# Kernel optimization log

Hardware: AMD Instinct MI355X
Metric: run time of the kernel (lower is better)

The kernel has to match this reference:

```python
import jax, jax.numpy as jnp
import numpy as np
from jax import lax

B, C1, IN_CH, OUT_CH, H1, W1 = 2, 64, 128, 64, 128, 128
BN_EPS = 1e-5


def conv3x3(x, w, b=None):
    # x: (N,C,H,W), w: (O,I,3,3), padding=1, stride=1 (matches nn.Conv2d)
    y = lax.conv_general_dilated(x, w, (1, 1), ((1, 1), (1, 1)),
                                 dimension_numbers=('NCHW', 'OIHW', 'NCHW'))
    return y if b is None else y + b[None, :, None, None]


def bn_relu(x, g, b):
    # training-mode BatchNorm2d (batch statistics over N,H,W) followed by ReLU
    m = x.mean((0, 2, 3), keepdims=True)
    v = x.var((0, 2, 3), keepdims=True)
    return jax.nn.relu((x - m) * lax.rsqrt(v + BN_EPS) * g[None, :, None, None]
                       + b[None, :, None, None])


def deform_offset(x, off_w):
    # ConvOffset2D: learn 2 offsets per pixel per channel, bilinear-gather input.
    Bc, C, H, W = x.shape
    offsets = conv3x3(x, off_w)                      # (B, 2C, H, W)
    off = offsets.reshape(Bc * C, H, W, 2)           # same flat reinterpretation as torch .view
    xf = x.reshape(Bc * C, H, W)
    gy, gx = jnp.meshgrid(jnp.arange(H, dtype=x.dtype),
                          jnp.arange(W, dtype=x.dtype), indexing='ij')
    cy = jnp.clip(off[..., 0] + gy, 0.0, H - 1)      # clamp per-axis like th_batch_map_coordinates
    cx = jnp.clip(off[..., 1] + gx, 0.0, W - 1)
    y0f, x0f = jnp.floor(cy), jnp.floor(cx)
    y0 = y0f.astype(jnp.int32); y1 = jnp.ceil(cy).astype(jnp.int32)
    x0 = x0f.astype(jnp.int32); x1c = jnp.ceil(cx).astype(jnp.int32)
    bidx = jnp.arange(Bc * C)[:, None, None]
    v00 = xf[bidx, y0, x0]; v10 = xf[bidx, y1, x0]
    v01 = xf[bidx, y0, x1c]; v11 = xf[bidx, y1, x1c]
    wy = cy - y0f; wx = cx - x0f
    vt = v00 + (v10 - v00) * wy                      # interp along H
    vb = v01 + (v11 - v01) * wy
    return (vt + (vb - vt) * wx).reshape(Bc, C, H, W)


def setup_inputs() -> dict:
    key = jax.random.key(0)
    ks = jax.random.split(key, 8)
    f = jnp.float32
    x1 = jax.random.normal(ks[0], (B, C1, H1, W1), f)
    x2 = jax.random.normal(ks[1], (B, C1, 2 * H1, 2 * W1), f)
    up_w = jax.random.normal(ks[2], (C1, C1, 2, 2), f) * 0.05   # torch IOHW layout
    up_b = jnp.zeros((C1,), f)
    off_w = jax.random.normal(ks[3], (2 * IN_CH, IN_CH, 3, 3), f) * 0.01  # init_normal_stddev
    c1_w = jax.random.normal(ks[4], (OUT_CH, IN_CH, 3, 3), f) * 0.05
    c1_b = jnp.zeros((OUT_CH,), f)
    g1 = jnp.ones((OUT_CH,), f); b1 = jnp.zeros((OUT_CH,), f)
    c2_w = jax.random.normal(ks[5], (OUT_CH, OUT_CH, 3, 3), f) * 0.05
    c2_b = jnp.zeros((OUT_CH,), f)
    g2 = jnp.ones((OUT_CH,), f); b2 = jnp.zeros((OUT_CH,), f)
    return dict(x1=x1, x2=x2, up_w=up_w, up_b=up_b, off_w=off_w,
                c1_w=c1_w, c1_b=c1_b, g1=g1, b1=b1,
                c2_w=c2_w, c2_b=c2_b, g2=g2, b2=b2)


def reference(x1, x2, up_w, up_b, off_w, c1_w, c1_b, g1, b1, c2_w, c2_b, g2, b2):
    # ConvTranspose2d(k=2, s=2): each input pixel expands to a 2x2 block
    Bx, Ci, H, W = x1.shape
    up = jnp.einsum('bihw,iokl->bohkwl', x1, up_w).reshape(Bx, up_w.shape[1], 2 * H, 2 * W)
    up = up + up_b[None, :, None, None]
    # pad skip connection to match (zero here; kept for faithfulness; torch pads W by diffX, H by diffY)
    dX = up.shape[2] - x2.shape[2]
    dY = up.shape[3] - x2.shape[3]
    x2p = jnp.pad(x2, ((0, 0), (0, 0), (dY // 2, dY // 2), (dX // 2, dX // 2)))
    xcat = jnp.concatenate([x2p, up], axis=1)        # (B, IN_CH, 2H, 2W)
    xd = deform_offset(xcat, off_w)
    h = bn_relu(conv3x3(xd, c1_w, c1_b), g1, b1)
    return bn_relu(conv3x3(h, c2_w, c2_b), g2, b2)
```

## Files before the change

### kernel.cpp

```cpp
#include <hip/hip_runtime.h>
#include <hip/hip_bf16.h>


typedef short short8 __attribute__((ext_vector_type(8)));
typedef short short4v __attribute__((ext_vector_type(4)));
typedef float f32x4 __attribute__((ext_vector_type(4)));

__device__ unsigned char g_ws[201u << 20] __attribute__((aligned(256)));
__device__ float g_st[256];

#define OFF_XCAT 0u
#define OFF_OFF  (36u << 20)
#define OFF_XD   (100u << 20)
#define OFF_C1O  (134u << 20)
#define OFF_H1   (150u << 20)
#define OFF_C2O  (168u << 20)
#define OFF_WO   (184u << 20)
#define OFF_W1   ((184u << 20) + 589824u)
#define OFF_W2   ((184u << 20) + 737280u)
#define OFF_XPU  (185u << 20)

#define XROW 264
#define XRSH (XROW * 128)

__device__ __forceinline__ float b2f(__hip_bfloat16 v) { return __bfloat162float(v); }
__device__ __forceinline__ short f2b(float v) {
  __hip_bfloat16 h = __float2bfloat16(v); short s; __builtin_memcpy(&s, &h, 2); return s;
}
__device__ __forceinline__ float s2f(short s) {
  __hip_bfloat16 h; __builtin_memcpy(&h, &s, 2); return __bfloat162float(h);
}
__device__ __forceinline__ void gload_lds16(const void* g, void* l) {
  __builtin_amdgcn_global_load_lds(
      (const __attribute__((address_space(1))) void*)g,
      (__attribute__((address_space(3))) void*)l, 16, 0, 0);
}

__device__ __forceinline__ void halo_zero(short* base, int C, int cshift, int u) {
  const int cg = u & ((1 << cshift) - 1);
  const int rest = u >> cshift;
  const int p = rest % 2576, b = rest / 2576;
  int row, col;
  if (p < 264) { row = 0; col = p; }
  else if (p < 528) { row = 257; col = p - 264; }
  else { int q = p - 528; row = 1 + (q >> 3); int cs = q & 7; col = cs ? 256 + cs : 0; }
  short8 z = {};
  *(short8*)(base + (((size_t)(b * 258) + row) * XROW + col) * C + cg * 8) = z;
}

__global__ __launch_bounds__(256)
void k_prep(const float* __restrict__ offw, const float* __restrict__ c1w,
            const float* __restrict__ c2w) {
  const int fid = blockIdx.x * 256 + threadIdx.x;
  if (blockIdx.x == 0) g_st[threadIdx.x] = 0.f;
  __hip_bfloat16* Wo = (__hip_bfloat16*)(g_ws + OFF_WO);
  __hip_bfloat16* W1 = (__hip_bfloat16*)(g_ws + OFF_W1);
  __hip_bfloat16* W2 = (__hip_bfloat16*)(g_ws + OFF_W2);
  if (fid < 294912) {
    int ic = fid & 127, rest = fid >> 7, oc = rest & 255, tap = rest >> 8;
    Wo[fid] = __float2bfloat16(offw[(oc * 128 + ic) * 9 + tap]);
  } else if (fid < 368640) {
    int l = fid - 294912;
    int ic = l & 127, rest = l >> 7, oc = rest & 63, tap = rest >> 6;
    W1[l] = __float2bfloat16(c1w[(oc * 128 + ic) * 9 + tap]);
  } else if (fid < 405504) {
    int l = fid - 368640;
    int ic = l & 63, rest = l >> 6, oc = rest & 63, tap = rest >> 6;
    W2[l] = __float2bfloat16(c2w[(oc * 64 + ic) * 9 + tap]);
  } else {
    int u = fid - 405504;
    if (u < 82432) halo_zero((short*)(g_ws + OFF_XCAT), 128, 4, u);
    else if (u < 164864) halo_zero((short*)(g_ws + OFF_XD), 128, 4, u - 82432);
    else halo_zero((short*)(g_ws + OFF_H1), 64, 3, u - 164864);
  }
}

__global__ __launch_bounds__(256)
void k_xpose(const float* __restrict__ x2) {
  __shared__ short T[256][72];
  const int t = threadIdx.x;
  const int h = blockIdx.x & 255, b = blockIdx.x >> 8;
  const float* src = x2 + (size_t)(b * 64) * 65536 + h * 256;
  for (int rep = 0; rep < 64; ++rep) {
    int flat = rep * 256 + t, c = flat >> 8, w = flat & 255;
    T[w][c] = f2b(src[(size_t)c * 65536 + w]);
  }
  __syncthreads();
  short* xcat = (short*)(g_ws + OFF_XCAT) +
                (((size_t)(b * 258) + h + 1) * XROW + 1) * 128;
  for (int rep = 0; rep < 8; ++rep) {
    int unit = rep * 256 + t;
    int w = unit >> 3, cg = unit & 7;
    *(short8*)(xcat + (size_t)w * 128 + cg * 8) = *(short8*)(&T[w][cg * 8]);
  }
}

__global__ __launch_bounds__(256)
void k_upmfma(const float* __restrict__ x1, const float* __restrict__ up_w,
              const float* __restrict__ up_b) {
  __shared__ short W4[4][64][66];
  __shared__ short X[64][68];
  __shared__ short U[2][128][66];
  __shared__ float BS[64];
  const int t = threadIdx.x;
  const int half = blockIdx.x & 1, hs = (blockIdx.x >> 1) & 127, b = blockIdx.x >> 8;
  for (int rep = 0; rep < 64; ++rep) {
    int flat = rep * 256 + t;
    int i = flat >> 8, rest = flat & 255, o = rest >> 2, kl = rest & 3;
    W4[kl][o][i] = f2b(up_w[flat]);
  }
  if (t < 64) BS[t] = up_b[t];
  const float* x1b = x1 + (size_t)(b * 64) * 16384 + hs * 128 + half * 64;
  for (int rep = 0; rep < 16; ++rep) {
    int flat = rep * 256 + t;
    int i = flat >> 6, ws = flat & 63;
    X[ws][i] = f2b(x1b[(size_t)i * 16384 + ws]);
  }
  __syncthreads();
  const int wv = t >> 6, lane = t & 63, l15 = lane & 15, quad = lane >> 4;
  short8 bf[2];
#pragma unroll
  for (int ks = 0; ks < 2; ++ks)
    bf[ks] = *(const short8*)(&X[wv * 16 + l15][ks * 32 + quad * 8]);
#pragma unroll
  for (int combo = 0; combo < 4; ++combo) {
    const int k = combo >> 1, l = combo & 1;
    f32x4 acc[4] = {};
#pragma unroll
    for (int nt = 0; nt < 4; ++nt)
#pragma unroll
      for (int ks = 0; ks < 2; ++ks) {
        short8 af = *(const short8*)(&W4[combo][nt * 16 + l15][ks * 32 + quad * 8]);
        acc[nt] = __builtin_amdgcn_mfma_f32_16x16x32_bf16(af, bf[ks], acc[nt], 0, 0, 0);
      }
    const int wl = 2 * (wv * 16 + l15) + l;
#pragma unroll
    for (int nt = 0; nt < 4; ++nt) {
      short4v s;
#pragma unroll
      for (int r = 0; r < 4; ++r) s[r] = f2b(acc[nt][r] + BS[nt * 16 + quad * 4 + r]);
      *(short4v*)(&U[k][wl][nt * 16 + quad * 4]) = s;
    }
  }
  __syncthreads();
  short* xcat = (short*)(g_ws + OFF_XCAT);
  short* xpu = (short*)(g_ws + OFF_XPU);
  for (int rep = 0; rep < 8; ++rep) {
    int unit = rep * 256 + t;
    int k = unit >> 10, wl = (unit >> 3) & 127, cg = unit & 7;
    int h = 2 * hs + k, w = half * 128 + wl;
    *(short8*)(xcat + (((size_t)(b * 258) + h + 1) * XROW + w + 1) * 128 + 64 + cg * 8) =
        *(short8*)(&U[k][wl][cg * 8]);
  }
  for (int rep = 0; rep < 8; ++rep) {
    int unit = rep * 256 + t;
    int o = unit >> 5, k = (unit >> 4) & 1, wg = unit & 15;
    int h = 2 * hs + k;
    short8 v;
#pragma unroll
    for (int j = 0; j < 8; ++j) v[j] = U[k][wg * 8 + j][o];
    *(short8*)(xpu + (size_t)(b * 64 + o) * 65536 + h * 256 + half * 128 + wg * 8) = v;
  }
}

__global__ __launch_bounds__(512, 2)
void k_offconv() {
  __shared__ short Bs[3 * 264 * 64];
  __shared__ short As0[256 * 32];
  __shared__ short As1[256 * 32];
  const short* X = (const short*)(g_ws + OFF_XCAT);
  const __hip_bfloat16* W = (const __hip_bfloat16*)(g_ws + OFF_WO);
  const int t = threadIdx.x;
  const int vb = (int)((blockIdx.x & 7) * 64 + (blockIdx.x >> 3));
  const int h = vb & 255, b = vb >> 8;
  const int wid = t >> 6, lane = t & 63, l15 = lane & 15, quad = lane >> 4;
  const int ocbase = (wid & 1) * 128;
  const int pxb = (wid >> 1) * 64;
  const int lpx = lane >> 3, lcg = lane & 7;
  const short* bsrc = X + (((size_t)(b * 258) + h) * XROW + lpx) * 128 + (lcg ^ (lpx & 7)) * 8;
  const int loc = lane >> 2, lcg4 = lane & 3;
  const __hip_bfloat16* asrc = W + (size_t)loc * 128 + (lcg4 ^ ((loc + (loc >> 2)) & 3)) * 8;
  const int ax = (quad ^ ((l15 + (l15 >> 2)) & 3)) << 3;
  const int abase = (ocbase + l15) * 32 + ax;
  f32x4 acc[8][4] = {};

#define STAGE_A(TAP, ICS, P, APTR)                                                  \
  {                                                                                 \
    _Pragma("unroll")                                                               \
    for (int k = 0; k < 2; ++k) {                                                   \
      int u = wid * 2 + k;                                                          \
      gload_lds16(asrc + ((size_t)(TAP) * 256 + u * 16) * 128 + (P) * 64 + (ICS) * 32, \
                  &APTR[u * 512]);                                                  \
    }                                                                               \
  }

  for (int p = 0; p < 2; ++p) {
    if (p) __syncthreads();
    for (int u = wid; u < 99; u += 8) {
      int r = u / 33, g = u - r * 33;
      gload_lds16(bsrc + (size_t)r * XRSH + g * 1024 + p * 64, &Bs[(r * 264 + g * 8) * 64]);
    }
    STAGE_A(0, 0, p, As0);
    STAGE_A(0, 1, p, As1);
    __syncthreads();
    for (int tap = 0; tap < 9; ++tap) {
      const int ky = tap / 3, kx = tap - 3 * ky;
      const short* srow = &Bs[(ky * 264 + pxb + l15 + kx) * 64];
      const int sx = ((l15 + kx) & 7) << 3;
      {
        short8 a[8], bf[4];
#pragma unroll
        for (int ot = 0; ot < 8; ++ot) a[ot] = *(const short8*)(As0 + abase + ot * 512);
#pragma unroll
        for (int pt = 0; pt < 4; ++pt)
          bf[pt] = *(const short8*)(srow + pt * 1024 + ((quad * 8) ^ sx));
        __syncthreads();
        if (tap < 8) STAGE_A(tap + 1, 0, p, As0);
#pragma unroll
        for (int ot = 0; ot < 8; ++ot)
#pragma unroll
          for (int pt = 0; pt < 4; ++pt)
            acc[ot][pt] = __builtin_amdgcn_mfma_f32_16x16x32_bf16(a[ot], bf[pt], acc[ot][pt], 0, 0, 0);
      }
      {
        short8 a[8], bf[4];
#pragma unroll
        for (int ot = 0; ot < 8; ++ot) a[ot] = *(const short8*)(As1 + abase + ot * 512);
#pragma unroll
        for (int pt = 0; pt < 4; ++pt)
          bf[pt] = *(const short8*)(srow + pt * 1024 + ((32 + quad * 8) ^ sx));
        __syncthreads();
        if (tap < 8) STAGE_A(tap + 1, 1, p, As1);
#pragma unroll
        for (int ot = 0; ot < 8; ++ot)
#pragma unroll
          for (int pt = 0; pt < 4; ++pt)
            acc[ot][pt] = __builtin_amdgcn_mfma_f32_16x16x32_bf16(a[ot], bf[pt], acc[ot][pt], 0, 0, 0);
      }
    }
  }
  __hip_bfloat16* out = (__hip_bfloat16*)(g_ws + OFF_OFF);
#pragma unroll
  for (int ot = 0; ot < 8; ++ot)
#pragma unroll
    for (int pt = 0; pt < 4; ++pt)
#pragma unroll
      for (int r = 0; r < 4; ++r) {
        int oc = ocbase + ot * 16 + quad * 4 + r;
        int px = pxb + pt * 16 + l15;
        out[(((size_t)(b * 256 + oc)) * 256 + h) * 256 + px] =
            __float2bfloat16(acc[ot][pt][r]);
      }
#undef STAGE_A
}

template <int IC, int SO>
__global__ __launch_bounds__(256, 2)
void k_conv(size_t xoff, size_t woff, const float* __restrict__ bias, size_t ooff) {
  __shared__ short Bs[3 * 272 * 32];
  __shared__ short As[2 * 2048];
  __shared__ float SB[128];
  const short* X = (const short*)(g_ws + xoff);
  const __hip_bfloat16* W = (const __hip_bfloat16*)(g_ws + woff);
  const int t = threadIdx.x;
  const int vb = (int)((blockIdx.x & 7) * 64 + (blockIdx.x >> 3));
  const int h = vb & 255, b = vb >> 8;
  const int wid = t >> 6, lane = t & 63, l15 = lane & 15, quad = lane >> 4;
  const int pxb = wid * 64;
  if (t < 128) SB[t] = 0.f;
  const int lpx = lane >> 2, lc = lane & 3;
  const int fl = (lpx + (lpx >> 2)) & 3;
  const short* bsrc = X + (((size_t)(b * 258) + h) * XROW + lpx) * IC + (lc ^ fl) * 8;
  const __hip_bfloat16* asrc = W + (size_t)lpx * IC + (lc ^ fl) * 8;
  const int aslot = (quad ^ ((l15 + (l15 >> 2)) & 3)) << 3;
  f32x4 acc[4][4] = {};
  const int KP = IC / 32;
  for (int ph = 0; ph < KP; ++ph) {
    for (int u = wid; u < 51; u += 4) {
      int r = u / 17, g = u - r * 17;
      gload_lds16(bsrc + ((size_t)r * XROW + g * 16) * IC + ph * 32,
                  &Bs[(r * 272 + g * 16) * 32]);
    }
    gload_lds16(asrc + (size_t)(wid * 16) * IC + ph * 32, &As[wid * 512]);
    __syncthreads();
    for (int tap = 0; tap < 9; ++tap) {
      short* Ac = &As[(tap & 1) * 2048];
      short* An = &As[((tap & 1) ^ 1) * 2048];
      if (tap < 8)
        gload_lds16(asrc + ((size_t)((tap + 1) * 64) + wid * 16) * IC + ph * 32,
                    &An[wid * 512]);
      const int ky = tap / 3, kx = tap - 3 * ky;
      short8 a[4], bf[4];
#pragma unroll
      for (int ot = 0; ot < 4; ++ot)
        a[ot] = *(const short8*)(&Ac[(ot * 16 + l15) * 32 + aslot]);
      const int s = l15 + kx;
      const int bslot = (quad ^ ((s + (s >> 2)) & 3)) << 3;
#pragma unroll
      for (int pt = 0; pt < 4; ++pt)
        bf[pt] = *(const short8*)(&Bs[(ky * 272 + pxb + pt * 16 + s) * 32 + bslot]);
#pragma unroll
      for (int ot = 0; ot < 4; ++ot)
#pragma unroll
        for (int pt = 0; pt < 4; ++pt)
          acc[ot][pt] = __builtin_amdgcn_mfma_f32_16x16x32_bf16(a[ot], bf[pt], acc[ot][pt], 0, 0, 0);
      __syncthreads();
    }
  }
  __hip_bfloat16* out = (__hip_bfloat16*)(g_ws + ooff);
#pragma unroll
  for (int ot = 0; ot < 4; ++ot) {
    const int oc0 = ot * 16 + quad * 4;
    float bv[4], sa[4] = {}, sa2[4] = {};
#pragma unroll
    for (int r = 0; r < 4; ++r) bv[r] = bias[oc0 + r];
#pragma unroll
    for (int pt = 0; pt < 4; ++pt) {
      const int px = pxb + pt * 16 + l15;
      short4v sv;
#pragma unroll
      for (int r = 0; r < 4; ++r) {
        float f = acc[ot][pt][r] + bv[r];
        sv[r] = f2b(f);
        sa[r] += f;
        sa2[r] = fmaf(f, f, sa2[r]);
      }
      *(short4v*)(out + ((((size_t)(b * 256) + h) * 256 + px) * 64 + oc0)) = sv;
    }
#pragma unroll
    for (int r = 0; r < 4; ++r) {
      float sv1 = sa[r], sv2 = sa2[r];
      for (int d = 1; d < 16; d <<= 1) {
        sv1 += __shfl_xor(sv1, d);
        sv2 += __shfl_xor(sv2, d);
      }
      if (l15 == 0) {
        atomicAdd(&SB[oc0 + r], sv1);
        atomicAdd(&SB[64 + oc0 + r], sv2);
      }
    }
  }
  __syncthreads();
  if (t < 128) atomicAdd(&g_st[SO + t], SB[t]);
}

__global__ __launch_bounds__(256, 4)
void k_gather(const float* __restrict__ x2) {
  __shared__ short G[256 * 66];
  const __hip_bfloat16* off = (const __hip_bfloat16*)(g_ws + OFF_OFF);
  const __hip_bfloat16* xpu = (const __hip_bfloat16*)(g_ws + OFF_XPU);
  short* xd = (short*)(g_ws + OFF_XD);
  const int t = threadIdx.x;
  const int half = blockIdx.x & 1;
  const int hh = (blockIdx.x >> 1) & 255, b = blockIdx.x >> 9;
  const int hp = 2 * (hh & 127) + (t >> 7);
  const int w0e = 2 * (t & 127);
  const int chb = hh >> 7;
  const int c0 = half * 64;
  const float fh = (float)hh, fw = (float)t;
  const __hip_bfloat16* offb = off + ((size_t)(b * 256) * 256 + hp) * 256 + w0e +
                               (size_t)(2 * c0 + chb) * 65536;
  if (half == 0) {
    const float* x2b = x2 + (size_t)b * 64 * 65536;
    for (int g4 = 0; g4 < 16; ++g4) {
      unsigned ovv[4];
#pragma unroll
      for (int j = 0; j < 4; ++j)
        ovv[j] = *(const unsigned*)(offb + (size_t)(2 * (g4 * 4 + j)) * 65536);
#pragma unroll
      for (int j = 0; j < 4; ++j) {
        const int crel = g4 * 4 + j;
        unsigned ov = ovv[j];
        float oy = __uint_as_float((ov & 0xffffu) << 16);
        float ox = __uint_as_float((ov >> 16) << 16);
        float cy = fminf(fmaxf(oy + fh, 0.f), 255.f);
        float cx = fminf(fmaxf(ox + fw, 0.f), 255.f);
        float y0f = floorf(cy), x0f = floorf(cx);
        int y0 = (int)y0f, x0 = (int)x0f;
        int y1 = (int)ceilf(cy), x1 = (int)ceilf(cx);
        const float* pl = x2b + (size_t)crel * 65536;
        float v00 = pl[y0 * 256 + x0], v10 = pl[y1 * 256 + x0];
        float v01 = pl[y0 * 256 + x1], v11 = pl[y1 * 256 + x1];
        float wy = cy - y0f, wx = cx - x0f;
        float vt = v00 + (v10 - v00) * wy;
        float vb = v01 + (v11 - v01) * wy;
        G[t * 66 + crel] = f2b(vt + (vb - vt) * wx);
      }
    }
  } else {
    const __hip_bfloat16* xub = xpu + (size_t)b * 64 * 65536;
    for (int g4 = 0; g4 < 16; ++g4) {
      unsigned ovv[4];
#pragma unroll
      for (int j = 0; j < 4; ++j)
        ovv[j] = *(const unsigned*)(offb + (size_t)(2 * (g4 * 4 + j)) * 65536);
#pragma unroll
      for (int j = 0; j < 4; ++j) {
        const int crel = g4 * 4 + j;
        unsigned ov = ovv[j];
        float oy = __uint_as_float((ov & 0xffffu) << 16);
        float ox = __uint_as_float((ov >> 16) << 16);
        float cy = fminf(fmaxf(oy + fh, 0.f), 255.f);
        float cx = fminf(fmaxf(ox + fw, 0.f), 255.f);
        float y0f = floorf(cy), x0f = floorf(cx);
        int y0 = (int)y0f, x0 = (int)x0f;
        int y1 = (int)ceilf(cy), x1 = (int)ceilf(cx);
        const __hip_bfloat16* pl = xub + (size_t)crel * 65536;
        float v00 = b2f(pl[y0 * 256 + x0]), v10 = b2f(pl[y1 * 256 + x0]);
        float v01 = b2f(pl[y0 * 256 + x1]), v11 = b2f(pl[y1 * 256 + x1]);
        float wy = cy - y0f, wx = cx - x0f;
        float vt = v00 + (v10 - v00) * wy;
        float vb = v01 + (v11 - v01) * wy;
        G[t * 66 + crel] = f2b(vt + (vb - vt) * wx);
      }
    }
  }
  __syncthreads();
  const size_t dst = (((size_t)(b * 258) + hh + 1) * XROW + 1) * 128 + c0;
  for (int it = 0; it < 8; ++it) {
    int g = it * 256 + t;
    *(short8*)(xd + dst + (size_t)(g >> 3) * 128 + (g & 7) * 8) =
        *(short8*)(&G[(g >> 3) * 66 + (g & 7) * 8]);
  }
}

__global__ __launch_bounds__(256)
void k_bnrelu1(const float* __restrict__ g, const float* __restrict__ be) {
  __shared__ float A[64], Bc[64];
  const __hip_bfloat16* x = (const __hip_bfloat16*)(g_ws + OFF_C1O);
  short* o = (short*)(g_ws + OFF_H1);
  const int t = threadIdx.x;
  const int h = blockIdx.x & 255, b = blockIdx.x >> 8;
  if (t < 64) {
    float m = g_st[t] * (1.f / 131072.f);
    float v = g_st[64 + t] * (1.f / 131072.f) - m * m;
    float iv = rsqrtf(v + 1e-5f) * g[t];
    A[t] = iv;
    Bc[t] = be[t] - m * iv;
  }
  __syncthreads();
  const __hip_bfloat16* px = x + (((size_t)(b * 256) + h) * 256 + t) * 64;
  short* op = o + (((size_t)(b * 258) + h + 1) * XROW + t + 1) * 64;
#pragma unroll
  for (int cg = 0; cg < 8; ++cg) {
    short8 v = *(const short8*)(px + cg * 8);
    short8 r;
#pragma unroll
    for (int j = 0; j < 8; ++j) {
      int c = cg * 8 + j;
      r[j] = f2b(fmaxf(s2f(v[j]) * A[c] + Bc[c], 0.f));
    }
    *(short8*)(op + cg * 8) = r;
  }
}

__global__ __launch_bounds__(256)
void k_bnrelu2(const float* __restrict__ g, const float* __restrict__ be,
               float* __restrict__ dout) {
  __shared__ float T[64 * 257];
  __shared__ float A[64], Bc[64];
  const __hip_bfloat16* x = (const __hip_bfloat16*)(g_ws + OFF_C2O);
  const int t = threadIdx.x;
  const int h = blockIdx.x & 255, b = blockIdx.x >> 8;
  if (t < 64) {
    float m = g_st[128 + t] * (1.f / 131072.f);
    float v = g_st[192 + t] * (1.f / 131072.f) - m * m;
    float iv = rsqrtf(v + 1e-5f) * g[t];
    A[t] = iv;
    Bc[t] = be[t] - m * iv;
  }
  __syncthreads();
  const __hip_bfloat16* px = x + (((size_t)(b * 256) + h) * 256 + t) * 64;
#pragma unroll
  for (int cg = 0; cg < 8; ++cg) {
    short8 v = *(const short8*)(px + cg * 8);
#pragma unroll
    for (int j = 0; j < 8; ++j) {
      int c = cg * 8 + j;
      T[c * 257 + t] = fmaxf(s2f(v[j]) * A[c] + Bc[c], 0.f);
    }
  }
  __syncthreads();
  for (int rep = 0; rep < 64; ++rep) {
    int flat = rep * 256 + t, c = flat >> 8, w = flat & 255;
    dout[(((size_t)(b * 64 + c)) * 256 + h) * 256 + w] = T[c * 257 + w];
  }
}

extern "C" void kernel_launch(void* const* d_in, const int* in_sizes, int n_in,
                              void* d_out, int out_size, void* d_ws, size_t ws_size,
                              hipStream_t stream) {
  const bool ok = (n_in == 13) &&
                  in_sizes[0] == 2097152 && in_sizes[1] == 8388608 &&
                  in_sizes[2] == 16384 && in_sizes[3] == 64 &&
                  in_sizes[4] == 294912 && in_sizes[5] == 73728 &&
                  in_sizes[9] == 36864 && out_size == 8388608;
  if (!ok) { hipMemsetAsync(d_out, 0x46, (size_t)out_size * 2, stream); return; }

  const float* x1   = (const float*)d_in[0];
  const float* x2   = (const float*)d_in[1];
  const float* up_w = (const float*)d_in[2];
  const float* up_b = (const float*)d_in[3];
  const float* offw = (const float*)d_in[4];
  const float* c1w  = (const float*)d_in[5];
  const float* c1b  = (const float*)d_in[6];
  const float* g1   = (const float*)d_in[7];
  const float* b1   = (const float*)d_in[8];
  const float* c2w  = (const float*)d_in[9];
  const float* c2b  = (const float*)d_in[10];
  const float* g2   = (const float*)d_in[11];
  const float* b2   = (const float*)d_in[12];

  k_prep<<<2389, 256, 0, stream>>>(offw, c1w, c2w);
  k_xpose<<<512, 256, 0, stream>>>(x2);
  k_upmfma<<<512, 256, 0, stream>>>(x1, up_w, up_b);
  k_offconv<<<512, 512, 0, stream>>>();
  k_gather<<<1024, 256, 0, stream>>>(x2);
  k_conv<128, 0><<<512, 256, 0, stream>>>(OFF_XD, OFF_W1, c1b, OFF_C1O);
  k_bnrelu1<<<512, 256, 0, stream>>>(g1, b1);
  k_conv<64, 128><<<512, 256, 0, stream>>>(OFF_H1, OFF_W2, c2b, OFF_C2O);
  k_bnrelu2<<<512, 256, 0, stream>>>(g2, b2, (float*)d_out);

  (void)d_ws; (void)ws_size;
}
```

Measured before the change: 340.6 us.

## Retile offset conv into smaller blocks with double-buffered weight staging

The offset convolution kernel drops from 512-thread blocks covering a full row and all 256 output channels to 256-thread blocks covering half a row and 128 channels, launched as 2048 blocks. The input-channel slice staged per phase shrinks to 32 (four phases), and weight tiles are now double-buffered across taps with one barrier per tap instead of two. The goal is higher occupancy (three blocks per CU) and less shared memory per block, so global-load latency overlaps better with MFMA work. The cost is more reloading of input rows and weights across blocks, and fewer MFMAs per LDS read.

Result: no change. 345.7 us (+1.5%).

```diff
diff --git a/kernel.cpp b/kernel.cpp
--- a/kernel.cpp
+++ b/kernel.cpp
@@ -163,95 +163,77 @@
   }
 }
 
-__global__ __launch_bounds__(512, 2)
+__global__ __launch_bounds__(256, 3)
 void k_offconv() {
-  __shared__ short Bs[3 * 264 * 64];
-  __shared__ short As0[256 * 32];
-  __shared__ short As1[256 * 32];
+  __shared__ short Bs[3 * 144 * 32];
+  __shared__ short As[2][4096];
   const short* X = (const short*)(g_ws + OFF_XCAT);
   const __hip_bfloat16* W = (const __hip_bfloat16*)(g_ws + OFF_WO);
   const int t = threadIdx.x;
-  const int vb = (int)((blockIdx.x & 7) * 64 + (blockIdx.x >> 3));
-  const int h = vb & 255, b = vb >> 8;
+  const int vb = (int)((blockIdx.x & 7) * 256 + (blockIdx.x >> 3));
+  const int ocb = vb & 1, wh = (vb >> 1) & 1, h = (vb >> 2) & 255, b = vb >> 10;
+  const int w0 = wh * 128, oc0blk = ocb * 128;
   const int wid = t >> 6, lane = t & 63, l15 = lane & 15, quad = lane >> 4;
-  const int ocbase = (wid & 1) * 128;
-  const int pxb = (wid >> 1) * 64;
-  const int lpx = lane >> 3, lcg = lane & 7;
-  const short* bsrc = X + (((size_t)(b * 258) + h) * XROW + lpx) * 128 + (lcg ^ (lpx & 7)) * 8;
-  const int loc = lane >> 2, lcg4 = lane & 3;
-  const __hip_bfloat16* asrc = W + (size_t)loc * 128 + (lcg4 ^ ((loc + (loc >> 2)) & 3)) * 8;
-  const int ax = (quad ^ ((l15 + (l15 >> 2)) & 3)) << 3;
-  const int abase = (ocbase + l15) * 32 + ax;
-  f32x4 acc[8][4] = {};
-
-#define STAGE_A(TAP, ICS, P, APTR)                                                  \
-  {                                                                                 \
-    _Pragma("unroll")                                                               \
-    for (int k = 0; k < 2; ++k) {                                                   \
-      int u = wid * 2 + k;                                                          \
-      gload_lds16(asrc + ((size_t)(TAP) * 256 + u * 16) * 128 + (P) * 64 + (ICS) * 32, \
-                  &APTR[u * 512]);                                                  \
-    }                                                                               \
-  }
-
-  for (int p = 0; p < 2; ++p) {
-    if (p) __syncthreads();
-    for (int u = wid; u < 99; u += 8) {
-      int r = u / 33, g = u - r * 33;
-      gload_lds16(bsrc + (size_t)r * XRSH + g * 1024 + p * 64, &Bs[(r * 264 + g * 8) * 64]);
-    }
-    STAGE_A(0, 0, p, As0);
-    STAGE_A(0, 1, p, As1);
+  const int ocw = wid & 1, pxw = wid >> 1;
+  const int lpx = lane >> 2, lc = lane & 3;
+  const int fl = (lpx + (lpx >> 2)) & 3;
+  const short* bsrc = X + (((size_t)(b * 258) + h) * XROW + w0 + lpx) * 128 + (lc ^ fl) * 8;
+  const __hip_bfloat16* asrc = W + (size_t)(oc0blk + lpx) * 128 + (lc ^ fl) * 8;
+  const int aslot = (quad ^ ((l15 + (l15 >> 2)) & 3)) << 3;
+  f32x4 acc[4][4] = {};
+  for (int ph = 0; ph < 4; ++ph) {
+    for (int u = wid; u < 27; u += 4) {
+      int r = u / 9, g = u - r * 9;
+      gload_lds16(bsrc + ((size_t)r * XROW + g * 16) * 128 + ph * 32,
+                  &Bs[(r * 144 + g * 16) * 32]);
+    }
+#pragma unroll
+    for (int k = 0; k < 2; ++k) {
+      int u = wid * 2 + k;
+      gload_lds16(asrc + (size_t)(u * 16) * 128 + ph * 32, &As[0][u * 512]);
+    }
     __syncthreads();
     for (int tap = 0; tap < 9; ++tap) {
+      const short* Ac = As[tap & 1];
+      short* An = As[(tap & 1) ^ 1];
+      if (tap < 8) {
+#pragma unroll
+        for (int k = 0; k < 2; ++k) {
+          int u = wid * 2 + k;
+          gload_lds16(asrc + ((size_t)((tap + 1) * 256) + u * 16) * 128 + ph * 32,
+                      &An[u * 512]);
+        }
+      }
       const int ky = tap / 3, kx = tap - 3 * ky;
-      const short* srow = &Bs[(ky * 264 + pxb + l15 + kx) * 64];
-      const int sx = ((l15 + kx) & 7) << 3;
-      {
-        short8 a[8], bf[4];
-#pragma unroll
-        for (int ot = 0; ot < 8; ++ot) a[ot] = *(const short8*)(As0 + abase + ot * 512);
+      short8 a[4], bf[4];
+#pragma unroll
+      for (int ot = 0; ot < 4; ++ot)
+        a[ot] = *(const short8*)(&Ac[(ocw * 64 + ot * 16 + l15) * 32 + aslot]);
+      const int s = l15 + kx;
+      const int bslot = (quad ^ ((s + (s >> 2)) & 3)) << 3;
+#pragma unroll
+      for (int pt = 0; pt < 4; ++pt)
+        bf[pt] = *(const short8*)(&Bs[(ky * 144 + pxw * 64 + pt * 16 + s) * 32 + bslot]);
+#pragma unroll
+      for (int ot = 0; ot < 4; ++ot)
 #pragma unroll
         for (int pt = 0; pt < 4; ++pt)
-          bf[pt] = *(const short8*)(srow + pt * 1024 + ((quad * 8) ^ sx));
-        __syncthreads();
-        if (tap < 8) STAGE_A(tap + 1, 0, p, As0);
-#pragma unroll
-        for (int ot = 0; ot < 8; ++ot)
-#pragma unroll
-          for (int pt = 0; pt < 4; ++pt)
-            acc[ot][pt] = __builtin_amdgcn_mfma_f32_16x16x32_bf16(a[ot], bf[pt], acc[ot][pt], 0, 0, 0);
-      }
-      {
-        short8 a[8], bf[4];
-#pragma unroll
-        for (int ot = 0; ot < 8; ++ot) a[ot] = *(const short8*)(As1 + abase + ot * 512);
-#pragma unroll
-        for (int pt = 0; pt < 4; ++pt)
-          bf[pt] = *(const short8*)(srow + pt * 1024 + ((32 + quad * 8) ^ sx));
-        __syncthreads();
-        if (tap < 8) STAGE_A(tap + 1, 1, p, As1);
-#pragma unroll
-        for (int ot = 0; ot < 8; ++ot)
-#pragma unroll
-          for (int pt = 0; pt < 4; ++pt)
-            acc[ot][pt] = __builtin_amdgcn_mfma_f32_16x16x32_bf16(a[ot], bf[pt], acc[ot][pt], 0, 0, 0);
-      }
+          acc[ot][pt] = __builtin_amdgcn_mfma_f32_16x16x32_bf16(a[ot], bf[pt], acc[ot][pt], 0, 0, 0);
+      __syncthreads();
     }
   }
   __hip_bfloat16* out = (__hip_bfloat16*)(g_ws + OFF_OFF);
 #pragma unroll
-  for (int ot = 0; ot < 8; ++ot)
+  for (int ot = 0; ot < 4; ++ot)
 #pragma unroll
     for (int pt = 0; pt < 4; ++pt)
 #pragma unroll
       for (int r = 0; r < 4; ++r) {
-        int oc = ocbase + ot * 16 + quad * 4 + r;
-        int px = pxb + pt * 16 + l15;
+        int oc = oc0blk + ocw * 64 + ot * 16 + quad * 4 + r;
+        int px = w0 + pxw * 64 + pt * 16 + l15;
         out[(((size_t)(b * 256 + oc)) * 256 + h) * 256 + px] =
             __float2bfloat16(acc[ot][pt][r]);
       }
-#undef STAGE_A
 }
 
 template <int IC, int SO>
@@ -514,7 +496,7 @@
   k_prep<<<2389, 256, 0, stream>>>(offw, c1w, c2w);
   k_xpose<<<512, 256, 0, stream>>>(x2);
   k_upmfma<<<512, 256, 0, stream>>>(x1, up_w, up_b);
-  k_offconv<<<512, 512, 0, stream>>>();
+  k_offconv<<<2048, 256, 0, stream>>>();
   k_gather<<<1024, 256, 0, stream>>>(x2);
   k_conv<128, 0><<<512, 256, 0, stream>>>(OFF_XD, OFF_W1, c1b, OFF_C1O);
   k_bnrelu1<<<512, 256, 0, stream>>>(g1, b1);
```
